# Kernel tuning notes

Hardware: AMD Instinct MI355X
Metric: run time of the kernel (lower is better)

## Reference

```python
import jax, jax.numpy as jnp
import numpy as np

EMBED = 512
MLP_DIM = 2048
B, T = 4, 4096
EPS = 1e-5


def setup_inputs() -> dict:
    key = jax.random.key(0)
    ks = jax.random.split(key, 8)
    s = lambda fan_in: 1.0 / np.sqrt(fan_in)
    inp = {
        "x": jax.random.normal(ks[0], (B, T, EMBED), dtype=jnp.float32),
        "Wq": jax.random.uniform(ks[1], (EMBED, EMBED), jnp.float32, -s(EMBED), s(EMBED)),
        "bq": jnp.zeros((EMBED,), jnp.float32),
        "Wk": jax.random.uniform(ks[2], (EMBED, EMBED), jnp.float32, -s(EMBED), s(EMBED)),
        "bk": jnp.zeros((EMBED,), jnp.float32),
        "Wv": jax.random.uniform(ks[3], (EMBED, EMBED), jnp.float32, -s(EMBED), s(EMBED)),
        "bv": jnp.zeros((EMBED,), jnp.float32),
        "W1": jax.random.uniform(ks[4], (EMBED, MLP_DIM), jnp.float32, -s(EMBED), s(EMBED)),
        "b1": jnp.zeros((MLP_DIM,), jnp.float32),
        "W2": jax.random.uniform(ks[5], (MLP_DIM, EMBED), jnp.float32, -s(MLP_DIM), s(MLP_DIM)),
        "b2": jnp.zeros((EMBED,), jnp.float32),
        "ln1_g": jnp.ones((EMBED,), jnp.float32),
        "ln1_b": jnp.zeros((EMBED,), jnp.float32),
        "ln2_g": jnp.ones((EMBED,), jnp.float32),
        "ln2_b": jnp.zeros((EMBED,), jnp.float32),
    }
    return inp


def _layernorm(x, g, b):
    mu = x.mean(-1, keepdims=True)
    var = ((x - mu) ** 2).mean(-1, keepdims=True)
    return (x - mu) * jax.lax.rsqrt(var + EPS) * g + b


def reference(x, Wq, bq, Wk, bk, Wv, bv, W1, b1, W2, b2, ln1_g, ln1_b, ln2_g, ln2_b):
    # pre-LN causal self-attention (single head)
    h = _layernorm(x, ln1_g, ln1_b)
    q = h @ Wq + bq  # [B,T,D]
    k = h @ Wk + bk
    v = h @ Wv + bv
    scale = 1.0 / jnp.sqrt(jnp.float32(EMBED))
    scores = jnp.einsum("btd,bsd->bts", q, k) * scale  # [B,T,T]
    mask = jnp.tril(jnp.ones((T, T), dtype=bool))
    scores = jnp.where(mask, scores, -jnp.inf)
    # NOTE: source applies softmax over the ENTIRE [T,T] matrix per batch
    # element (global max + global sum), not per-row. Replicate exactly.
    m = scores.max(axis=(-2, -1), keepdims=True)
    e = jnp.exp(scores - m)
    attn = e / e.sum(axis=(-2, -1), keepdims=True)
    x = x + jnp.einsum("bts,bsd->btd", attn, v)
    # MLP
    h2 = _layernorm(x, ln2_g, ln2_b)
    x = x + (jax.nn.gelu(h2 @ W1 + b1, approximate=False) @ W2 + b2)
    return x
```

## Files before the change

kernel.cpp:

```cpp
#include <hip/hip_runtime.h>
#include <hip/hip_bf16.h>
#include <math.h>

#define EMBED 512
#define MLPD  2048
#define NB    4
#define TS    4096
#define BT    (NB*TS)
#define BK    64
#define NTILES_TRI 528

typedef __attribute__((ext_vector_type(4))) float f32x4;
typedef __attribute__((ext_vector_type(8))) short s16x8;
typedef __hip_bfloat16 bf16_t;

__device__ __forceinline__ void gload16(const void* g, void* l) {
  __builtin_amdgcn_global_load_lds(
      (const __attribute__((address_space(1))) void*)g,
      (__attribute__((address_space(3))) void*)l, 16, 0, 0);
}

__device__ __forceinline__ float fast_erf(float y) {
  const float ay = fabsf(y);
  const float t = __builtin_amdgcn_rcpf(1.0f + 0.3275911f*ay);
  float poly = 1.061405429f;
  poly = poly*t - 1.453152027f;
  poly = poly*t + 1.421413741f;
  poly = poly*t - 0.284496736f;
  poly = poly*t + 0.254829592f;
  poly = poly*t;
  const float e = 1.0f - poly*__expf(-ay*ay);
  return copysignf(e, y);
}


__device__ __forceinline__ void gemm_core(
    const bf16_t* __restrict__ A, int lda,
    const bf16_t* __restrict__ Bt, int ldb,
    int kmax, bf16_t* Alds, bf16_t* Blds, f32x4 acc[4][4])
{
  const int tid = threadIdx.x;
  const int w  = tid >> 6;
  const int l  = tid & 63;
  const int wr = w >> 1, wc = w & 1;
  const int fr = l & 15, fg = l >> 4;

  #pragma unroll
  for (int i = 0; i < 4; ++i)
    #pragma unroll
    for (int j = 0; j < 4; ++j)
      #pragma unroll
      for (int e = 0; e < 4; ++e)
        acc[i][j][e] = 0.0f;

  const int srow = w*32 + (l >> 3);
  const int sx = (((l & 7) ^ ((l >> 3) & 7)))*8;
  const int rsw = fr & 7;

  for (int k0 = 0; k0 < kmax; k0 += BK) {
    __syncthreads();
    #pragma unroll
    for (int c = 0; c < 4; ++c) {
      const bf16_t* ga = A  + (size_t)(srow + c*8)*lda + (k0 + sx);
      const bf16_t* gb = Bt + (size_t)(srow + c*8)*ldb + (k0 + sx);
      gload16(ga, Alds + (w*32 + c*8)*BK);
      gload16(gb, Blds + (w*32 + c*8)*BK);
    }
    __syncthreads();
    #pragma unroll
    for (int kk = 0; kk < BK; kk += 32) {
      s16x8 av[4], bv[4];
      const int ch = (kk >> 3) + fg;
      const int co = (ch ^ rsw) << 3;
      #pragma unroll
      for (int mf = 0; mf < 4; ++mf)
        av[mf] = *(const s16x8*)(Alds + (wr*64 + mf*16 + fr)*BK + co);
      #pragma unroll
      for (int nf = 0; nf < 4; ++nf)
        bv[nf] = *(const s16x8*)(Blds + (wc*64 + nf*16 + fr)*BK + co);
      #pragma unroll
      for (int mf = 0; mf < 4; ++mf)
        #pragma unroll
        for (int nf = 0; nf < 4; ++nf)
          acc[mf][nf] = __builtin_amdgcn_mfma_f32_16x16x32_bf16(
              av[mf], bv[nf], acc[mf][nf], 0, 0, 0);
    }
  }
}

__device__ __forceinline__ void gemm_core_deep(
    const bf16_t* __restrict__ A, int lda,
    const bf16_t* __restrict__ Bt, int ldb,
    int kmax, bf16_t* Alds, bf16_t* Blds, f32x4 acc[4][4])
{
  const int tid = threadIdx.x;
  const int w  = tid >> 6;
  const int l  = tid & 63;
  const int wr = w >> 1, wc = w & 1;
  const int fr = l & 15, fg = l >> 4;

  #pragma unroll
  for (int i = 0; i < 4; ++i)
    #pragma unroll
    for (int j = 0; j < 4; ++j)
      #pragma unroll
      for (int e = 0; e < 4; ++e)
        acc[i][j][e] = 0.0f;

  const int srow = w*32 + (l >> 3);
  const int sx = (((l & 7) ^ ((l >> 3) & 7)))*8;
  const int rsw = fr & 7;
  const int T = kmax >> 6;

  #define ISSUE_A(t_) do { \
    bf16_t* dst = Alds + ((t_) % 3)*(128*BK); \
    const int k0_ = (t_)*BK; \
    _Pragma("unroll") \
    for (int c = 0; c < 4; ++c) \
      gload16(A + (size_t)(srow + c*8)*lda + (k0_ + sx), dst + (w*32 + c*8)*BK); \
  } while (0)
  #define ISSUE_B(t_) do { \
    bf16_t* dst = Blds + ((t_) & 1)*(128*BK); \
    const int k0_ = (t_)*BK; \
    _Pragma("unroll") \
    for (int c = 0; c < 4; ++c) \
      gload16(Bt + (size_t)(srow + c*8)*ldb + (k0_ + sx), dst + (w*32 + c*8)*BK); \
  } while (0)

  ISSUE_A(0); ISSUE_B(0);
  if (T > 1) ISSUE_A(1);

  for (int t = 0; t < T; ++t) {
    if (t <= T - 3) {
      ISSUE_B(t + 1); ISSUE_A(t + 2);
      asm volatile("s_waitcnt vmcnt(12)" ::: "memory");
    } else if (t == T - 2) {
      ISSUE_B(t + 1);
      asm volatile("s_waitcnt vmcnt(8)" ::: "memory");
    } else {
      asm volatile("s_waitcnt vmcnt(0)" ::: "memory");
    }
    __builtin_amdgcn_s_barrier();
    bf16_t* Ac = Alds + (t % 3)*(128*BK);
    bf16_t* Bc = Blds + (t & 1)*(128*BK);
    #pragma unroll
    for (int kk = 0; kk < BK; kk += 32) {
      s16x8 av[4], bv[4];
      const int ch = (kk >> 3) + fg;
      const int co = (ch ^ rsw) << 3;
      #pragma unroll
      for (int mf = 0; mf < 4; ++mf)
        av[mf] = *(const s16x8*)(Ac + (wr*64 + mf*16 + fr)*BK + co);
      #pragma unroll
      for (int nf = 0; nf < 4; ++nf)
        bv[nf] = *(const s16x8*)(Bc + (wc*64 + nf*16 + fr)*BK + co);
      #pragma unroll
      for (int mf = 0; mf < 4; ++mf)
        #pragma unroll
        for (int nf = 0; nf < 4; ++nf)
          acc[mf][nf] = __builtin_amdgcn_mfma_f32_16x16x32_bf16(
              av[mf], bv[nf], acc[mf][nf], 0, 0, 0);
    }
    __builtin_amdgcn_s_barrier();
  }
  #undef ISSUE_A
  #undef ISSUE_B
}

#define EPILOGUE_SETUP \
  const int l = threadIdx.x & 63; const int w = threadIdx.x >> 6; \
  const int wr = w >> 1, wc = w & 1, fr = l & 15, fg = l >> 4;

__global__ void __launch_bounds__(256) k_proj_qkv(
    const bf16_t* __restrict__ A,
    const bf16_t* __restrict__ wqt, const bf16_t* __restrict__ wkt,
    const bf16_t* __restrict__ wvt,
    const float* __restrict__ bq, const float* __restrict__ bk,
    const float* __restrict__ bv,
    bf16_t* __restrict__ qb, bf16_t* __restrict__ kb, bf16_t* __restrict__ vt)
{
  __shared__ __align__(16) bf16_t Alds[128*BK];
  __shared__ __align__(16) bf16_t Blds[128*BK];
  f32x4 acc[4][4];
  const int z = blockIdx.z;
  const bf16_t* Wt = (z == 0) ? wqt : (z == 1) ? wkt : wvt;
  const float* bias = (z == 0) ? bq : (z == 1) ? bk : bv;
  const int m0 = blockIdx.x*128, n0 = blockIdx.y*128;
  gemm_core(A + (size_t)m0*EMBED, EMBED, Wt + (size_t)n0*EMBED, EMBED, EMBED,
            Alds, Blds, acc);
  EPILOGUE_SETUP
  if (z < 2) {
    bf16_t* outp = (z == 0) ? qb : kb;
    #pragma unroll
    for (int mf = 0; mf < 4; ++mf)
      #pragma unroll
      for (int nf = 0; nf < 4; ++nf) {
        const int col = n0 + wc*64 + nf*16 + fr;
        const float bb = bias[col];
        #pragma unroll
        for (int j = 0; j < 4; ++j) {
          const int row = m0 + wr*64 + mf*16 + fg*4 + j;
          outp[(size_t)row*EMBED + col] = __float2bfloat16(acc[mf][nf][j] + bb);
        }
      }
  } else {
    #pragma unroll
    for (int mf = 0; mf < 4; ++mf)
      #pragma unroll
      for (int nf = 0; nf < 4; ++nf) {
        const int col = n0 + wc*64 + nf*16 + fr;
        const float bb = bias[col];
        #pragma unroll
        for (int j = 0; j < 4; ++j) {
          const int row = m0 + wr*64 + mf*16 + fg*4 + j;
          const int b = row >> 12, t = row & 4095;
          vt[((size_t)b*EMBED + col)*TS + t] = __float2bfloat16(acc[mf][nf][j] + bb);
        }
      }
  }
}

__global__ void __launch_bounds__(256) k_attn1(
    const bf16_t* __restrict__ q, const bf16_t* __restrict__ kmat,
    bf16_t* __restrict__ P, float* __restrict__ partials, int serial_b)
{
  __shared__ __align__(16) bf16_t LB[2][128*BK];
  bf16_t* Alds = LB[0];
  bf16_t* Blds = LB[1];
  bf16_t* Plds = &LB[0][0];
  int b, r;
  if (serial_b >= 0) {
    b = serial_b; r = blockIdx.x;
  } else {
    const int L = blockIdx.x;
    const int logical = (L & 7)*264 + (L >> 3);
    b = logical / NTILES_TRI;
    r = logical - b*NTILES_TRI;
  }
  int ti = (int)((sqrtf(8.0f*(float)r + 1.0f) - 1.0f)*0.5f);
  while ((ti + 1)*(ti + 2)/2 <= r) ++ti;
  while (ti*(ti + 1)/2 > r) --ti;
  const int tj = r - ti*(ti + 1)/2;

  f32x4 acc[4][4];
  const bf16_t* A  = q    + ((size_t)b*TS + (size_t)ti*128)*EMBED;
  const bf16_t* Bt = kmat + ((size_t)b*TS + (size_t)tj*128)*EMBED;
  gemm_core(A, EMBED, Bt, EMBED, EMBED, Alds, Blds, acc);

  EPILOGUE_SETUP
  __syncthreads();
  const float SC = 0.044194173824159216f;
  float lsum = 0.0f;
  #pragma unroll
  for (int mf = 0; mf < 4; ++mf)
    #pragma unroll
    for (int nf = 0; nf < 4; ++nf) {
      const int ls = wc*64 + nf*16 + fr;
      const int gs = tj*128 + ls;
      #pragma unroll
      for (int j = 0; j < 4; ++j) {
        const int lt = wr*64 + mf*16 + fg*4 + j;
        const int gt = ti*128 + lt;
        float e = 0.0f;
        if (gs <= gt) e = __expf(acc[mf][nf][j]*SC - 30.0f);
        const int sc = (((ls >> 3) ^ (lt & 7)) << 3) | (ls & 7);
        Plds[lt*128 + sc] = __float2bfloat16(e);
        lsum += e;
      }
    }
  __syncthreads();
  bf16_t* Pb = P + (size_t)((serial_b >= 0) ? 0 : b)*TS*TS
                 + (size_t)ti*128*TS + tj*128;
  #pragma unroll
  for (int it = 0; it < 8; ++it) {
    const int row = w*32 + it*4 + (l >> 4);
    const int ch  = l & 15;
    const int chs2 = (ch & 8) | ((ch ^ (row & 7)) & 7);
    const s16x8 v = *(const s16x8*)(Plds + row*128 + chs2*8);
    *(s16x8*)(Pb + (size_t)row*TS + ch*8) = v;
  }
  #pragma unroll
  for (int off = 32; off > 0; off >>= 1) lsum += __shfl_xor(lsum, off);
  __shared__ float red[4];
  if (l == 0) red[w] = lsum;
  __syncthreads();
  if (threadIdx.x == 0)
    partials[(size_t)b*NTILES_TRI + r] = red[0] + red[1] + red[2] + red[3];
}

__global__ void k_reduce(const float* __restrict__ part, float* __restrict__ S, int n)
{
  const int b = blockIdx.x;
  const int l = threadIdx.x;
  float s = 0.0f;
  for (int i = l; i < n; i += 64) s += part[(size_t)b*n + i];
  #pragma unroll
  for (int off = 32; off > 0; off >>= 1) s += __shfl_xor(s, off);
  if (l == 0) S[b] = s;
}

__global__ void __launch_bounds__(256) k_attn2(
    const bf16_t* __restrict__ P, const bf16_t* __restrict__ vt,
    const float* __restrict__ S, const float* __restrict__ x,
    float* __restrict__ out, int serial_b)
{
  __shared__ __align__(16) bf16_t Alds[3*128*BK];
  __shared__ __align__(16) bf16_t Blds[2*128*BK];
  int ti, nj, b;
  if (serial_b >= 0) {
    ti = blockIdx.x; nj = blockIdx.y; b = serial_b;
  } else {
    const int L = blockIdx.x;
    const int xc = L & 7;
    const int idx = L >> 3;
    nj = idx & 3;
    const int s = idx >> 2;
    b = s & 3;
    const int which = s >> 2;
    ti = (which == 0) ? 2*xc
       : (which == 1) ? 2*xc + 1
       : (which == 2) ? 30 - 2*xc
                      : 31 - 2*xc;
  }
  f32x4 acc[4][4];
  const bf16_t* A  = P + (size_t)((serial_b >= 0) ? 0 : b)*TS*TS + (size_t)ti*128*TS;
  const bf16_t* Bt = vt + ((size_t)b*EMBED + (size_t)nj*128)*TS;
  const int kmax = (ti + 1)*128;
  gemm_core_deep(A, TS, Bt, TS, kmax, Alds, Blds, acc);

  EPILOGUE_SETUP
  const float invS = 1.0f / S[b];
  #pragma unroll
  for (int mf = 0; mf < 4; ++mf)
    #pragma unroll
    for (int nf = 0; nf < 4; ++nf) {
      const int d = nj*128 + wc*64 + nf*16 + fr;
      #pragma unroll
      for (int j = 0; j < 4; ++j) {
        const int t = ti*128 + wr*64 + mf*16 + fg*4 + j;
        const size_t idx2 = ((size_t)b*TS + t)*EMBED + d;
        out[idx2] = x[idx2] + acc[mf][nf][j]*invS;
      }
    }
}

__global__ void __launch_bounds__(256) k_mlp1(
    const bf16_t* __restrict__ A, const bf16_t* __restrict__ Wt,
    const float* __restrict__ bias, bf16_t* __restrict__ mid)
{
  __shared__ __align__(16) bf16_t Alds[3*128*BK];
  __shared__ __align__(16) bf16_t Blds[2*128*BK];
  f32x4 acc[4][4];
  const int m0 = blockIdx.x*128, n0 = blockIdx.y*128;
  gemm_core_deep(A + (size_t)m0*EMBED, EMBED, Wt + (size_t)n0*EMBED, EMBED, EMBED,
                 Alds, Blds, acc);
  EPILOGUE_SETUP
  bf16_t* Plds = Alds;
  __syncthreads();
  #pragma unroll
  for (int mf = 0; mf < 4; ++mf)
    #pragma unroll
    for (int nf = 0; nf < 4; ++nf) {
      const int ls = wc*64 + nf*16 + fr;
      const float bb = bias[n0 + ls];
      #pragma unroll
      for (int j = 0; j < 4; ++j) {
        const int lt = wr*64 + mf*16 + fg*4 + j;
        const float pre = acc[mf][nf][j] + bb;
        const float ge = 0.5f*pre*(1.0f + fast_erf(pre*0.70710678118654752f));
        const int sc = (((ls >> 3) ^ (lt & 7)) << 3) | (ls & 7);
        Plds[lt*128 + sc] = __float2bfloat16(ge);
      }
    }
  __syncthreads();
  bf16_t* Mb = mid + (size_t)m0*MLPD + n0;
  #pragma unroll
  for (int it = 0; it < 8; ++it) {
    const int row = w*32 + it*4 + (l >> 4);
    const int ch  = l & 15;
    const int chs2 = (ch & 8) | ((ch ^ (row & 7)) & 7);
    const s16x8 v = *(const s16x8*)(Plds + row*128 + chs2*8);
    *(s16x8*)(Mb + (size_t)row*MLPD + ch*8) = v;
  }
}

__global__ void __launch_bounds__(256) k_mlp2(
    const bf16_t* __restrict__ A, const bf16_t* __restrict__ Wt,
    const float* __restrict__ bias, float* __restrict__ out)
{
  __shared__ __align__(16) bf16_t Alds[3*128*BK];
  __shared__ __align__(16) bf16_t Blds[2*128*BK];
  f32x4 acc[4][4];
  const int m0 = blockIdx.x*128, n0 = blockIdx.y*128;
  gemm_core_deep(A + (size_t)m0*MLPD, MLPD, Wt + (size_t)n0*MLPD, MLPD, MLPD,
                 Alds, Blds, acc);
  EPILOGUE_SETUP
  #pragma unroll
  for (int mf = 0; mf < 4; ++mf)
    #pragma unroll
    for (int nf = 0; nf < 4; ++nf) {
      const int col = n0 + wc*64 + nf*16 + fr;
      const float bb = bias[col];
      #pragma unroll
      for (int j = 0; j < 4; ++j) {
        const int row = m0 + wr*64 + mf*16 + fg*4 + j;
        const size_t idx = (size_t)row*EMBED + col;
        out[idx] = out[idx] + acc[mf][nf][j] + bb;
      }
    }
}

__global__ void __launch_bounds__(256) k_ln(
    const float* __restrict__ x, const float* __restrict__ g,
    const float* __restrict__ bta, bf16_t* __restrict__ h)
{
  const int row = blockIdx.x*4 + (threadIdx.x >> 6);
  const int l = threadIdx.x & 63;
  const float4* xr = (const float4*)(x + (size_t)row*EMBED);
  const float4 a = xr[l*2], c = xr[l*2 + 1];
  float vals[8] = {a.x, a.y, a.z, a.w, c.x, c.y, c.z, c.w};
  float s = 0.0f, ss = 0.0f;
  #pragma unroll
  for (int i = 0; i < 8; ++i) { s += vals[i]; ss += vals[i]*vals[i]; }
  #pragma unroll
  for (int off = 32; off > 0; off >>= 1) {
    s  += __shfl_xor(s,  off);
    ss += __shfl_xor(ss, off);
  }
  const float mu = s*(1.0f/EMBED);
  const float var = ss*(1.0f/EMBED) - mu*mu;
  const float rs = rsqrtf(var + 1e-5f);
  const float4* g4 = (const float4*)g;
  const float4* b4 = (const float4*)bta;
  const float4 ga = g4[l*2], gc = g4[l*2 + 1];
  const float4 ba = b4[l*2], bc = b4[l*2 + 1];
  const float gv[8] = {ga.x, ga.y, ga.z, ga.w, gc.x, gc.y, gc.z, gc.w};
  const float bv[8] = {ba.x, ba.y, ba.z, ba.w, bc.x, bc.y, bc.z, bc.w};
  s16x8 ov;
  bf16_t* ovp = (bf16_t*)&ov;
  #pragma unroll
  for (int i = 0; i < 8; ++i)
    ovp[i] = __float2bfloat16((vals[i] - mu)*rs*gv[i] + bv[i]);
  *((s16x8*)(h + (size_t)row*EMBED) + l) = ov;
}

__global__ void __launch_bounds__(256) k_transpose_all(
    const float* __restrict__ Wq, const float* __restrict__ Wk,
    const float* __restrict__ Wv, const float* __restrict__ W1,
    const float* __restrict__ W2,
    bf16_t* __restrict__ wqt, bf16_t* __restrict__ wkt,
    bf16_t* __restrict__ wvt, bf16_t* __restrict__ w1t,
    bf16_t* __restrict__ w2t)
{
  __shared__ float tile[32][33];
  int L = blockIdx.x;
  const float* W; bf16_t* Wt; int Kd, Nd, t;
  if (L < 768) {
    const int m = L >> 8; t = L & 255;
    W  = (m == 0) ? Wq : (m == 1) ? Wk : Wv;
    Wt = (m == 0) ? wqt : (m == 1) ? wkt : wvt;
    Kd = EMBED; Nd = EMBED;
  } else if (L < 1792) {
    t = L - 768;  W = W1; Wt = w1t; Kd = EMBED; Nd = MLPD;
  } else {
    t = L - 1792; W = W2; Wt = w2t; Kd = MLPD; Nd = EMBED;
  }
  const int ntx = Nd >> 5;
  const int tx32 = (t % ntx)*32, ty32 = (t / ntx)*32;
  const int x = threadIdx.x & 31, y8 = threadIdx.x >> 5;
  #pragma unroll
  for (int r = 0; r < 4; ++r) {
    const int y = y8 + r*8;
    tile[y][x] = W[(size_t)(ty32 + y)*Nd + tx32 + x];
  }
  __syncthreads();
  #pragma unroll
  for (int r = 0; r < 4; ++r) {
    const int y = y8 + r*8;
    Wt[(size_t)(tx32 + y)*Kd + ty32 + x] = __float2bfloat16(tile[x][y]);
  }
}

extern "C" void kernel_launch(void* const* d_in, const int* in_sizes, int n_in,
                              void* d_out, int out_size, void* d_ws, size_t ws_size,
                              hipStream_t stream) {
  (void)in_sizes; (void)n_in; (void)out_size;
  const float* x   = (const float*)d_in[0];
  const float* Wq  = (const float*)d_in[1];
  const float* bq  = (const float*)d_in[2];
  const float* Wk  = (const float*)d_in[3];
  const float* bk  = (const float*)d_in[4];
  const float* Wv  = (const float*)d_in[5];
  const float* bv  = (const float*)d_in[6];
  const float* W1  = (const float*)d_in[7];
  const float* b1  = (const float*)d_in[8];
  const float* W2  = (const float*)d_in[9];
  const float* b2  = (const float*)d_in[10];
  const float* g1  = (const float*)d_in[11];
  const float* be1 = (const float*)d_in[12];
  const float* g2  = (const float*)d_in[13];
  const float* be2 = (const float*)d_in[14];
  float* out = (float*)d_out;

  char* p = (char*)d_ws;
  auto alloc = [&](size_t bytes) -> char* {
    char* r = p; p += (bytes + 255) & ~(size_t)255; return r;
  };
  bf16_t* h   = (bf16_t*)alloc((size_t)BT*EMBED*2);
  bf16_t* wqt = (bf16_t*)alloc((size_t)EMBED*EMBED*2);
  bf16_t* wkt = (bf16_t*)alloc((size_t)EMBED*EMBED*2);
  bf16_t* wvt = (bf16_t*)alloc((size_t)EMBED*EMBED*2);
  bf16_t* w1t = (bf16_t*)alloc((size_t)MLPD*EMBED*2);
  bf16_t* w2t = (bf16_t*)alloc((size_t)EMBED*MLPD*2);
  bf16_t* qb  = (bf16_t*)alloc((size_t)BT*EMBED*2);
  bf16_t* kb  = (bf16_t*)alloc((size_t)BT*EMBED*2);
  bf16_t* vtb = (bf16_t*)alloc((size_t)BT*EMBED*2);
  float* partials = (float*)alloc((size_t)NB*NTILES_TRI*sizeof(float));
  float* S = (float*)alloc(256);

  const size_t mid_bytes = (size_t)BT*MLPD*2;
  const size_t p_full    = (size_t)NB*TS*TS*2;
  const size_t used = (size_t)(p - (char*)d_ws);
  const bool full = ws_size >= used + (p_full > mid_bytes ? p_full : mid_bytes);
  char* region = alloc(full ? p_full : mid_bytes);
  bf16_t* P   = (bf16_t*)region;
  bf16_t* mid = (bf16_t*)region;

  k_transpose_all<<<dim3(2816), 256, 0, stream>>>(Wq, Wk, Wv, W1, W2,
                                                  wqt, wkt, wvt, w1t, w2t);
  k_ln<<<BT/4, 256, 0, stream>>>(x, g1, be1, h);

  k_proj_qkv<<<dim3(BT/128, EMBED/128, 3), 256, 0, stream>>>(
      h, wqt, wkt, wvt, bq, bk, bv, qb, kb, vtb);

  if (full) {
    k_attn1<<<dim3(NB*NTILES_TRI), 256, 0, stream>>>(qb, kb, P, partials, -1);
    k_reduce<<<NB, 64, 0, stream>>>(partials, S, NTILES_TRI);
    k_attn2<<<dim3(512), 256, 0, stream>>>(P, vtb, S, x, out, -1);
  } else {
    for (int b = 0; b < NB; ++b) {
      k_attn1<<<dim3(NTILES_TRI), 256, 0, stream>>>(qb, kb, P, partials, b);
      k_reduce<<<1, 64, 0, stream>>>(partials + (size_t)b*NTILES_TRI, S + b, NTILES_TRI);
      k_attn2<<<dim3(TS/128, EMBED/128), 256, 0, stream>>>(P, vtb, S, x, out, b);
    }
  }

  k_ln<<<BT/4, 256, 0, stream>>>(out, g2, be2, h);
  k_mlp1<<<dim3(BT/128, MLPD/128), 256, 0, stream>>>(h, w1t, b1, mid);
  k_mlp2<<<dim3(BT/128, EMBED/128), 256, 0, stream>>>(mid, w2t, b2, out);
}
```

Baseline: 329.0 us.

## Use 256x256 tiles with 512 threads and triple-buffered BK32 pipeline for MLP1

```diff
diff --git a/kernel.cpp b/kernel.cpp
--- a/kernel.cpp
+++ b/kernel.cpp
@@ -8,6 +8,7 @@
 #define TS    4096
 #define BT    (NB*TS)
 #define BK    64
+#define BK2   32
 #define NTILES_TRI 528
 
 typedef __attribute__((ext_vector_type(4))) float f32x4;
@@ -32,7 +33,6 @@
   const float e = 1.0f - poly*__expf(-ay*ay);
   return copysignf(e, y);
 }
-
 
 __device__ __forceinline__ void gemm_core(
     const bf16_t* __restrict__ A, int lda,
@@ -165,6 +165,76 @@
   }
   #undef ISSUE_A
   #undef ISSUE_B
+}
+
+__device__ __forceinline__ void gemm256_core(
+    const bf16_t* __restrict__ A, int lda,
+    const bf16_t* __restrict__ Bt, int ldb,
+    int kmax, bf16_t* Alds, bf16_t* Blds, f32x4 acc[8][4])
+{
+  const int tid = threadIdx.x;
+  const int w  = tid >> 6;
+  const int l  = tid & 63;
+  const int wm = w >> 2, wn = w & 3;
+  const int fr = l & 15, fg = l >> 4;
+
+  #pragma unroll
+  for (int i = 0; i < 8; ++i)
+    #pragma unroll
+    for (int j = 0; j < 4; ++j)
+      #pragma unroll
+      for (int e = 0; e < 4; ++e)
+        acc[i][j][e] = 0.0f;
+
+  const int srow = l >> 2;
+  const int sx = ((l & 3) ^ ((l >> 3) & 3))*8;
+  const int rsw = (fr >> 1) & 3;
+  const int T = kmax / BK2;
+
+  #define ISS2(t_) do { \
+    bf16_t* da = Alds + ((t_) % 3)*(256*BK2); \
+    bf16_t* db = Blds + ((t_) % 3)*(256*BK2); \
+    const int k0_ = (t_)*BK2; \
+    _Pragma("unroll") \
+    for (int p = 0; p < 2; ++p) { \
+      gload16(A  + (size_t)(p*128 + w*16 + srow)*lda + (k0_ + sx), \
+              da + (p*128 + w*16)*BK2); \
+      gload16(Bt + (size_t)(p*128 + w*16 + srow)*ldb + (k0_ + sx), \
+              db + (p*128 + w*16)*BK2); \
+    } \
+  } while (0)
+
+  ISS2(0); ISS2(1);
+
+  for (int t = 0; t < T; ++t) {
+    if (t + 2 < T) {
+      ISS2(t + 2);
+      asm volatile("s_waitcnt vmcnt(8)" ::: "memory");
+    } else if (t + 1 < T) {
+      asm volatile("s_waitcnt vmcnt(4)" ::: "memory");
+    } else {
+      asm volatile("s_waitcnt vmcnt(0)" ::: "memory");
+    }
+    __builtin_amdgcn_s_barrier();
+    const bf16_t* Ac = Alds + (t % 3)*(256*BK2);
+    const bf16_t* Bc = Blds + (t % 3)*(256*BK2);
+    const int co = (fg ^ rsw)*8;
+    s16x8 av[8], bv[4];
+    #pragma unroll
+    for (int mf = 0; mf < 8; ++mf)
+      av[mf] = *(const s16x8*)(Ac + (wm*128 + mf*16 + fr)*BK2 + co);
+    #pragma unroll
+    for (int nf = 0; nf < 4; ++nf)
+      bv[nf] = *(const s16x8*)(Bc + (wn*64 + nf*16 + fr)*BK2 + co);
+    #pragma unroll
+    for (int mf = 0; mf < 8; ++mf)
+      #pragma unroll
+      for (int nf = 0; nf < 4; ++nf)
+        acc[mf][nf] = __builtin_amdgcn_mfma_f32_16x16x32_bf16(
+            av[mf], bv[nf], acc[mf][nf], 0, 0, 0);
+    __builtin_amdgcn_s_barrier();
+  }
+  #undef ISS2
 }
 
 #define EPILOGUE_SETUP \
@@ -344,44 +414,32 @@
     }
 }
 
-__global__ void __launch_bounds__(256) k_mlp1(
+__global__ void __launch_bounds__(512, 2) k_mlp1(
     const bf16_t* __restrict__ A, const bf16_t* __restrict__ Wt,
     const float* __restrict__ bias, bf16_t* __restrict__ mid)
 {
-  __shared__ __align__(16) bf16_t Alds[3*128*BK];
-  __shared__ __align__(16) bf16_t Blds[2*128*BK];
-  f32x4 acc[4][4];
-  const int m0 = blockIdx.x*128, n0 = blockIdx.y*128;
-  gemm_core_deep(A + (size_t)m0*EMBED, EMBED, Wt + (size_t)n0*EMBED, EMBED, EMBED,
-                 Alds, Blds, acc);
-  EPILOGUE_SETUP
-  bf16_t* Plds = Alds;
-  __syncthreads();
-  #pragma unroll
-  for (int mf = 0; mf < 4; ++mf)
+  __shared__ __align__(16) bf16_t Alds[3*256*BK2];
+  __shared__ __align__(16) bf16_t Blds[3*256*BK2];
+  f32x4 acc[8][4];
+  const int m0 = blockIdx.x*256, n0 = blockIdx.y*256;
+  gemm256_core(A + (size_t)m0*EMBED, EMBED, Wt + (size_t)n0*EMBED, EMBED, EMBED,
+               Alds, Blds, acc);
+  const int l = threadIdx.x & 63, w = threadIdx.x >> 6;
+  const int wm = w >> 2, wn = w & 3, fr = l & 15, fg = l >> 4;
+  #pragma unroll
+  for (int mf = 0; mf < 8; ++mf)
     #pragma unroll
     for (int nf = 0; nf < 4; ++nf) {
-      const int ls = wc*64 + nf*16 + fr;
-      const float bb = bias[n0 + ls];
+      const int col = n0 + wn*64 + nf*16 + fr;
+      const float bb = bias[col];
       #pragma unroll
       for (int j = 0; j < 4; ++j) {
-        const int lt = wr*64 + mf*16 + fg*4 + j;
+        const int row = m0 + wm*128 + mf*16 + fg*4 + j;
         const float pre = acc[mf][nf][j] + bb;
         const float ge = 0.5f*pre*(1.0f + fast_erf(pre*0.70710678118654752f));
-        const int sc = (((ls >> 3) ^ (lt & 7)) << 3) | (ls & 7);
-        Plds[lt*128 + sc] = __float2bfloat16(ge);
+        mid[(size_t)row*MLPD + col] = __float2bfloat16(ge);
       }
     }
-  __syncthreads();
-  bf16_t* Mb = mid + (size_t)m0*MLPD + n0;
-  #pragma unroll
-  for (int it = 0; it < 8; ++it) {
-    const int row = w*32 + it*4 + (l >> 4);
-    const int ch  = l & 15;
-    const int chs2 = (ch & 8) | ((ch ^ (row & 7)) & 7);
-    const s16x8 v = *(const s16x8*)(Plds + row*128 + chs2*8);
-    *(s16x8*)(Mb + (size_t)row*MLPD + ch*8) = v;
-  }
 }
 
 __global__ void __launch_bounds__(256) k_mlp2(
@@ -546,6 +604,6 @@
   }
 
   k_ln<<<BT/4, 256, 0, stream>>>(out, g2, be2, h);
-  k_mlp1<<<dim3(BT/128, MLPD/128), 256, 0, stream>>>(h, w1t, b1, mid);
+  k_mlp1<<<dim3(BT/256, MLPD/256), 512, 0, stream>>>(h, w1t, b1, mid);
   k_mlp2<<<dim3(BT/128, EMBED/128), 256, 0, stream>>>(mid, w2t, b2, out);
 }
```

New measurement: 299.4 us. 1.1x faster.
